# Kernel tuning notes

Hardware: AMD Instinct MI355X
Metric: run time of the kernel (lower is better)

Reference implementation:

```python
import math
import jax, jax.numpy as jnp
import numpy as np

B, T, D, H, L = 8, 512, 128, 128, 2
W_SCALE = 0.05  # xavier-like small init to keep exp() input gate numerically sane


def setup_inputs() -> dict:
    key = jax.random.key(0)
    ks = jax.random.split(key, 14)
    inp = {"x": jax.random.normal(ks[0], (B, T, D), jnp.float32)}
    names_w = ["Wq", "Wk", "Wv", "Wi", "Wf", "Wo"]
    for j, nm in enumerate(names_w):
        inp[nm] = jax.random.normal(ks[1 + j], (L, H, D), jnp.float32) * W_SCALE
    # q/k/v biases zero-initialized per reset_parameters; gate biases random
    inp["bq"] = jnp.zeros((L, H), jnp.float32)
    inp["bk"] = jnp.zeros((L, H), jnp.float32)
    inp["bv"] = jnp.zeros((L, H), jnp.float32)
    inp["bi"] = jax.random.normal(ks[7], (L, H), jnp.float32) * W_SCALE
    inp["bf"] = jax.random.normal(ks[8], (L, H), jnp.float32) * W_SCALE
    inp["bo"] = jax.random.normal(ks[9], (L, H), jnp.float32) * W_SCALE
    return inp


def _mlstm_layer(xin, Wq, bq, Wk, bk, Wv, bv, Wi, bi, Wf, bf, Wo, bo):
    # xin: (B, T, Din). Precompute all 6 projections for the full sequence.
    q = jnp.einsum("btd,hd->bth", xin, Wq) + bq
    k = (jnp.einsum("btd,hd->bth", xin, Wk) + bk) * (1.0 / math.sqrt(H))
    v = jnp.einsum("btd,hd->bth", xin, Wv) + bv
    i = jnp.exp(jnp.einsum("btd,hd->bth", xin, Wi) + bi)
    f = jax.nn.sigmoid(jnp.einsum("btd,hd->bth", xin, Wf) + bf)
    o = jax.nn.sigmoid(jnp.einsum("btd,hd->bth", xin, Wo) + bo)

    def step(carry, qkvifo):
        C, n = carry                      # C: (B,H,H), n: (B,H)
        qt, kt, vt, it, ft, ot = qkvifo   # each (B,H)
        h_tilde = jnp.einsum("bij,bj->bi", C, qt)
        denom = jnp.maximum(jnp.abs(jnp.einsum("bi,bi->b", n, qt)), 1.0)[:, None]
        h = ot * (h_tilde / denom)
        n_new = ft * n + it * kt
        C_new = ft[:, :, None] * C + it[:, :, None] * (vt[:, :, None] * kt[:, None, :])
        return (C_new, n_new), h

    Bc = xin.shape[0]
    C0 = jnp.zeros((Bc, H, H), xin.dtype)
    n0 = jnp.zeros((Bc, H), xin.dtype)
    seq = tuple(jnp.swapaxes(a, 0, 1) for a in (q, k, v, i, f, o))  # (T,B,H)
    _, hs = jax.lax.scan(step, (C0, n0), seq)
    return jnp.swapaxes(hs, 0, 1)  # (B,T,H)


def reference(x, Wq, bq, Wk, bk, Wv, bv, Wi, bi, Wf, bf, Wo, bo):
    h = x
    for l in range(L):  # small fixed layer loop (dropout=0.0 -> identity)
        h = _mlstm_layer(h, Wq[l], bq[l], Wk[l], bk[l], Wv[l], bv[l],
                         Wi[l], bi[l], Wf[l], bf[l], Wo[l], bo[l])
    return h  # (B, T, H) output sequence of last layer
```

## Files before the change

kernel.cpp:

```cpp
#include <hip/hip_runtime.h>
#include <math.h>

#define BB 8
#define TT 512
#define DD 128
#define HH 128
#define BT_ (BB * TT)
#define CL 32
#define NCH 16
static const size_t BTH = (size_t)BT_ * HH;


struct WArgs { const float* W[6]; };
struct BArgs { const float* b[6]; };

template <int CTRL>
__device__ __forceinline__ float dpp_add(float x) {
  int y = __builtin_amdgcn_update_dpp(0, __builtin_bit_cast(int, x), CTRL,
                                      0xF, 0xF, true);
  return x + __builtin_bit_cast(float, y);
}

__global__ __launch_bounds__(256)
void transpose_w(WArgs w, float* __restrict__ Wt) {
  __shared__ float t[32][33];
  const int l = blockIdx.y / 6, p = blockIdx.y % 6;
  const float* src = w.W[p] + (size_t)l * HH * DD;
  float* dst = Wt + (size_t)blockIdx.y * HH * DD;
  const int ty0 = (blockIdx.x >> 2) * 32, tx0 = (blockIdx.x & 3) * 32;
  const int tx = threadIdx.x & 31, ty = threadIdx.x >> 5;
#pragma unroll
  for (int j = 0; j < 32; j += 8)
    t[ty + j][tx] = src[(size_t)(ty0 + ty + j) * DD + tx0 + tx];
  __syncthreads();
#pragma unroll
  for (int j = 0; j < 32; j += 8)
    dst[(size_t)(tx0 + ty + j) * HH + ty0 + tx] = t[tx][ty + j];
}

__global__ __launch_bounds__(256)
void proj_kernel(const float* __restrict__ X, const float* __restrict__ Wtl,
                 BArgs args, float* __restrict__ act) {
  __shared__ float xs[64][132];
  const int p = blockIdx.y;
  const int row0 = blockIdx.x * 64;
  const int tid = threadIdx.x;
  {
    const float4* xg = (const float4*)(X + (size_t)row0 * DD);
#pragma unroll
    for (int i = 0; i < 8; ++i) {
      int u = tid + 256 * i;
      float4 v = xg[u];
      *(float4*)&xs[u >> 5][(u & 31) * 4] = v;
    }
  }
  __syncthreads();

  const int h0 = (tid & 15) * 8;
  const int r0 = (tid >> 4) * 4;
  const float* wtp = Wtl + (size_t)p * HH * DD;

  float acc[4][8];
#pragma unroll
  for (int r = 0; r < 4; ++r)
#pragma unroll
    for (int j = 0; j < 8; ++j) acc[r][j] = 0.f;

  for (int d0 = 0; d0 < DD; d0 += 4) {
    float4 wa[4], wb[4];
#pragma unroll
    for (int i = 0; i < 4; ++i) {
      wa[i] = *(const float4*)(wtp + (size_t)(d0 + i) * HH + h0);
      wb[i] = *(const float4*)(wtp + (size_t)(d0 + i) * HH + h0 + 4);
    }
    float4 xr[4];
#pragma unroll
    for (int r = 0; r < 4; ++r) xr[r] = *(const float4*)&xs[r0 + r][d0];
#pragma unroll
    for (int i = 0; i < 4; ++i) {
#pragma unroll
      for (int r = 0; r < 4; ++r) {
        const float xv = (i == 0) ? xr[r].x
                        : (i == 1) ? xr[r].y
                        : (i == 2) ? xr[r].z : xr[r].w;
        acc[r][0] = fmaf(xv, wa[i].x, acc[r][0]);
        acc[r][1] = fmaf(xv, wa[i].y, acc[r][1]);
        acc[r][2] = fmaf(xv, wa[i].z, acc[r][2]);
        acc[r][3] = fmaf(xv, wa[i].w, acc[r][3]);
        acc[r][4] = fmaf(xv, wb[i].x, acc[r][4]);
        acc[r][5] = fmaf(xv, wb[i].y, acc[r][5]);
        acc[r][6] = fmaf(xv, wb[i].z, acc[r][6]);
        acc[r][7] = fmaf(xv, wb[i].w, acc[r][7]);
      }
    }
  }

  const float4 b0 = *(const float4*)(args.b[p] + h0);
  const float4 b1 = *(const float4*)(args.b[p] + h0 + 4);
  const float bias[8] = {b0.x, b0.y, b0.z, b0.w, b1.x, b1.y, b1.z, b1.w};
#pragma unroll
  for (int r = 0; r < 4; ++r) {
    const size_t row = (size_t)row0 + r0 + r;
    float v[8];
#pragma unroll
    for (int j = 0; j < 8; ++j) {
      float a = acc[r][j] + bias[j];
      if (p == 1)      a *= 0.088388347648318447f;
      else if (p == 3) a = __expf(a);
      else if (p >= 4) a = 1.0f / (1.0f + __expf(-a));
      v[j] = a;
    }
    if (p == 0) {
      float* dst = act + row * HH + h0;
      *(float4*)dst = make_float4(v[0], v[1], v[2], v[3]);
      *(float4*)(dst + 4) = make_float4(v[4], v[5], v[6], v[7]);
    } else if (p == 1) {
      float* dst = act + BTH + row * HH + h0;
      *(float4*)dst = make_float4(v[0], v[1], v[2], v[3]);
      *(float4*)(dst + 4) = make_float4(v[4], v[5], v[6], v[7]);
    } else if (p == 3 || p == 4) {
      float* dst = act + 2 * BTH + row * 2 * HH + 2 * h0 + (p == 3 ? 0 : 1);
#pragma unroll
      for (int j = 0; j < 8; ++j) dst[2 * j] = v[j];
    } else {
      float* dst = act + 4 * BTH + row * 2 * HH + 2 * h0 + (p == 2 ? 0 : 1);
#pragma unroll
      for (int j = 0; j < 8; ++j) dst[2 * j] = v[j];
    }
  }
}

__global__ __launch_bounds__(512)
void cseg2_kernel(const float* __restrict__ act, float* __restrict__ cbuf,
                  float* __restrict__ abuf, float* __restrict__ nbufB) {
  __shared__ __align__(16) float kt[CL][128];
  __shared__ __align__(16) float ift[CL][64];
  __shared__ __align__(16) float vot[CL][64];
  const int tid = threadIdx.x;
  const int lane = tid & 63, wid = tid >> 6;
  const int blk = blockIdx.x;
  const int b = blk & 7, ch = (blk >> 3) & (NCH - 1), qtr = blk >> 7;
  const int t0 = ch * CL;
  const int p0 = qtr * 32;
  const size_t boff = (size_t)b * TT * HH;
  const float* kg = act + BTH + boff;
  const float* ifg = act + 2 * BTH + 2 * boff;
  const float* vog = act + 4 * BTH + 2 * boff;

#pragma unroll
  for (int i = 0; i < CL / 16; ++i) {
    const int u = tid + 512 * i;
    const int r = u >> 5, c = (u & 31) * 4;
    *(float4*)&kt[r][c] = *(const float4*)(kg + (size_t)(t0 + r) * HH + c);
  }
  {
    const int r = tid >> 4, c = (tid & 15) * 4;
    *(float4*)&ift[r][c] =
        *(const float4*)(ifg + (size_t)(t0 + r) * 2 * HH + 2 * p0 + c);
    *(float4*)&vot[r][c] =
        *(const float4*)(vog + (size_t)(t0 + r) * 2 * HH + 2 * p0 + c);
  }
  __syncthreads();

  const int pl = lane >> 4, cl = lane & 15;
  const int plocal = wid * 4 + pl;
  const int p = p0 + plocal;

  float C[8];
#pragma unroll
  for (int j = 0; j < 8; ++j) C[j] = 0.f;
  float Af = 1.f, Bn = 0.f;

#pragma unroll 4
  for (int t = 0; t < CL; ++t) {
    const float2 gif = *(const float2*)&ift[t][2 * plocal];
    const float2 gvo = *(const float2*)&vot[t][2 * plocal];
    const float4 k0 = *(const float4*)&kt[t][cl * 4];
    const float4 k1 = *(const float4*)&kt[t][cl * 4 + 64];
    const float kp = kt[t][p];
    const float a = gif.x * gvo.x;
    const float f = gif.y;
    C[0] = fmaf(f, C[0], a * k0.x);
    C[1] = fmaf(f, C[1], a * k0.y);
    C[2] = fmaf(f, C[2], a * k0.z);
    C[3] = fmaf(f, C[3], a * k0.w);
    C[4] = fmaf(f, C[4], a * k1.x);
    C[5] = fmaf(f, C[5], a * k1.y);
    C[6] = fmaf(f, C[6], a * k1.z);
    C[7] = fmaf(f, C[7], a * k1.w);
    Af *= f;
    Bn = fmaf(f, Bn, gif.x * kp);
  }

  const size_t slot = (size_t)(b * 128 + p) * NCH + ch;
  *(float4*)(cbuf + slot * 128 + cl * 4) = make_float4(C[0], C[1], C[2], C[3]);
  *(float4*)(cbuf + slot * 128 + cl * 4 + 64) =
      make_float4(C[4], C[5], C[6], C[7]);
  if (cl == 0) {
    abuf[slot] = Af;
    nbufB[slot] = Bn;
  }
}

__global__ __launch_bounds__(128)
void ndenom_kernel(float* __restrict__ act, const float* __restrict__ abuf,
                   const float* __restrict__ nbufB) {
  __shared__ float plds[8][132];
  __shared__ float den[8];
  const int b = blockIdx.x & 7, ch = blockIdx.x >> 3;
  const int p = threadIdx.x;
  const size_t boff = (size_t)b * TT * HH;
  const float* qp = act + boff + p;
  const float* kp = act + BTH + boff + p;
  const float* ifp = act + 2 * BTH + 2 * boff + 2 * p;
  float* vop = act + 4 * BTH + 2 * boff;
  const size_t cb = (size_t)(b * 128 + p) * NCH;

  float n = 0.f;
#pragma unroll 1
  for (int g = 0; g < ch; ++g) n = fmaf(abuf[cb + g], n, nbufB[cb + g]);

#pragma unroll 1
  for (int grp = 0; grp < CL / 8; ++grp) {
    const int t0 = ch * CL + grp * 8;
    float prod[8];
#pragma unroll
    for (int j = 0; j < 8; ++j) {
      const float2 iff = *(const float2*)(ifp + (size_t)(t0 + j) * 2 * HH);
      const float kv = kp[(size_t)(t0 + j) * HH];
      const float qv = qp[(size_t)(t0 + j) * HH];
      prod[j] = n * qv;
      n = fmaf(iff.y, n, iff.x * kv);
    }
#pragma unroll
    for (int j = 0; j < 8; ++j) plds[j][p] = prod[j];
    __syncthreads();
    {
      const int j = p >> 4, c = p & 15;
      const float4 a = *(const float4*)&plds[j][c * 8];
      const float4 d = *(const float4*)&plds[j][c * 8 + 4];
      float s = ((a.x + a.y) + (a.z + a.w)) + ((d.x + d.y) + (d.z + d.w));
      s = dpp_add<0x111>(s);
      s = dpp_add<0x112>(s);
      s = dpp_add<0x114>(s);
      s = dpp_add<0x118>(s);
      if ((p & 15) == 15)
        den[j] = __builtin_amdgcn_rcpf(fmaxf(fabsf(s), 1.0f));
    }
    __syncthreads();
#pragma unroll
    for (int j = 0; j < 8; ++j)
      vop[(size_t)(t0 + j) * 2 * HH + 2 * p + 1] *= den[j];
  }
}

__global__ __launch_bounds__(512)
void hscan2_kernel(const float* __restrict__ act, float* __restrict__ hout,
                   const float* __restrict__ cbuf,
                   const float* __restrict__ abuf) {
  __shared__ __align__(16) float qt[CL][128];
  __shared__ __align__(16) float kt[CL][128];
  __shared__ __align__(16) float ift[CL][64];
  __shared__ __align__(16) float vot[CL][64];
  const int tid = threadIdx.x;
  const int lane = tid & 63, wid = tid >> 6;
  const int blk = blockIdx.x;
  const int b = blk & 7, ch = (blk >> 3) & (NCH - 1), qtr = blk >> 7;
  const int t0 = ch * CL;
  const int p0 = qtr * 32;
  const size_t boff = (size_t)b * TT * HH;
  const float* qg = act + boff;
  const float* kg = act + BTH + boff;
  const float* ifg = act + 2 * BTH + 2 * boff;
  const float* vog = act + 4 * BTH + 2 * boff;

#pragma unroll
  for (int i = 0; i < CL / 16; ++i) {
    const int u = tid + 512 * i;
    const int r = u >> 5, c = (u & 31) * 4;
    *(float4*)&qt[r][c] = *(const float4*)(qg + (size_t)(t0 + r) * HH + c);
    *(float4*)&kt[r][c] = *(const float4*)(kg + (size_t)(t0 + r) * HH + c);
  }
  {
    const int r = tid >> 4, c = (tid & 15) * 4;
    *(float4*)&ift[r][c] =
        *(const float4*)(ifg + (size_t)(t0 + r) * 2 * HH + 2 * p0 + c);
    *(float4*)&vot[r][c] =
        *(const float4*)(vog + (size_t)(t0 + r) * 2 * HH + 2 * p0 + c);
  }
  __syncthreads();

  const int pl = lane >> 4, cl = lane & 15;
  const int plocal = wid * 4 + pl;
  const int p = p0 + plocal;

  float C[8];
#pragma unroll
  for (int j = 0; j < 8; ++j) C[j] = 0.f;
  {
    const size_t cb = (size_t)(b * 128 + p) * NCH;
#pragma unroll 1
    for (int g = 0; g < ch; ++g) {
      const float a = abuf[cb + g];
      const float4 b0 = *(const float4*)(cbuf + (cb + g) * 128 + cl * 4);
      const float4 b1 = *(const float4*)(cbuf + (cb + g) * 128 + cl * 4 + 64);
      C[0] = fmaf(a, C[0], b0.x);
      C[1] = fmaf(a, C[1], b0.y);
      C[2] = fmaf(a, C[2], b0.z);
      C[3] = fmaf(a, C[3], b0.w);
      C[4] = fmaf(a, C[4], b1.x);
      C[5] = fmaf(a, C[5], b1.y);
      C[6] = fmaf(a, C[6], b1.z);
      C[7] = fmaf(a, C[7], b1.w);
    }
  }
  float* hbase = hout + boff + p;

#pragma unroll 4
  for (int t = 0; t < CL; ++t) {
    const float2 gif = *(const float2*)&ift[t][2 * plocal];
    const float2 gvo = *(const float2*)&vot[t][2 * plocal];
    const float4 q0 = *(const float4*)&qt[t][cl * 4];
    const float4 q1 = *(const float4*)&qt[t][cl * 4 + 64];
    const float4 k0 = *(const float4*)&kt[t][cl * 4];
    const float4 k1 = *(const float4*)&kt[t][cl * 4 + 64];
    float s0 = C[0] * q0.x;
    float s1 = C[4] * q1.x;
    s0 = fmaf(C[1], q0.y, s0);
    s1 = fmaf(C[5], q1.y, s1);
    s0 = fmaf(C[2], q0.z, s0);
    s1 = fmaf(C[6], q1.z, s1);
    s0 = fmaf(C[3], q0.w, s0);
    s1 = fmaf(C[7], q1.w, s1);
    float s = s0 + s1;
    const float a = gif.x * gvo.x;
    const float f = gif.y;
    C[0] = fmaf(f, C[0], a * k0.x);
    C[1] = fmaf(f, C[1], a * k0.y);
    C[2] = fmaf(f, C[2], a * k0.z);
    C[3] = fmaf(f, C[3], a * k0.w);
    C[4] = fmaf(f, C[4], a * k1.x);
    C[5] = fmaf(f, C[5], a * k1.y);
    C[6] = fmaf(f, C[6], a * k1.z);
    C[7] = fmaf(f, C[7], a * k1.w);
    s = dpp_add<0x111>(s);
    s = dpp_add<0x112>(s);
    s = dpp_add<0x114>(s);
    s = dpp_add<0x118>(s);
    if (cl == 15) hbase[(size_t)(t0 + t) * HH] = s * gvo.y;
  }
}

extern "C" void kernel_launch(void* const* d_in, const int* in_sizes, int n_in,
                              void* d_out, int out_size, void* d_ws,
                              size_t ws_size, hipStream_t stream) {
  (void)in_sizes; (void)n_in; (void)out_size; (void)ws_size;
  const float* x = (const float*)d_in[0];
  float* act = (float*)d_ws;
  float* hbuf = act + 6 * BTH;
  float* cbuf = act + 7 * BTH;
  float* abuf = cbuf + (size_t)1024 * NCH * 128;
  float* nbufB = abuf + (size_t)1024 * NCH;
  float* Wt = (float*)d_out;

  WArgs wa;
  for (int j = 0; j < 6; ++j) wa.W[j] = (const float*)d_in[1 + j];
  transpose_w<<<dim3(16, 12), 256, 0, stream>>>(wa, Wt);

  for (int l = 0; l < 2; ++l) {
    BArgs ba;
    for (int j = 0; j < 6; ++j)
      ba.b[j] = (const float*)d_in[7 + j] + (size_t)l * HH;
    const float* wtl = Wt + (size_t)l * 6 * HH * DD;
    const float* xin = (l == 0) ? x : hbuf;
    float* hdst = (l == 0) ? hbuf : (float*)d_out;
    proj_kernel<<<dim3(BT_ / 64, 6), 256, 0, stream>>>(xin, wtl, ba, act);
    cseg2_kernel<<<512, 512, 0, stream>>>(act, cbuf, abuf, nbufB);
    ndenom_kernel<<<128, 128, 0, stream>>>(act, abuf, nbufB);
    hscan2_kernel<<<512, 512, 0, stream>>>(act, hdst, cbuf, abuf);
  }
}
```

Baseline: 205.0 us.

## Fold normalizer denominator computation into the h-scan kernel

```diff
diff --git a/kernel.cpp b/kernel.cpp
--- a/kernel.cpp
+++ b/kernel.cpp
@@ -132,7 +132,8 @@
 
 __global__ __launch_bounds__(512)
 void cseg2_kernel(const float* __restrict__ act, float* __restrict__ cbuf,
-                  float* __restrict__ abuf, float* __restrict__ nbufB) {
+                  float* __restrict__ abuf, float* __restrict__ nbufB,
+                  float* __restrict__ segA8, float* __restrict__ segB8) {
   __shared__ __align__(16) float kt[CL][128];
   __shared__ __align__(16) float ift[CL][64];
   __shared__ __align__(16) float vot[CL][64];
@@ -169,7 +170,7 @@
   float C[8];
 #pragma unroll
   for (int j = 0; j < 8; ++j) C[j] = 0.f;
-  float Af = 1.f, Bn = 0.f;
+  float Af = 1.f, Bn = 0.f, Aw = 1.f, Bw = 0.f;
 
 #pragma unroll 4
   for (int t = 0; t < CL; ++t) {
@@ -190,6 +191,17 @@
     C[7] = fmaf(f, C[7], a * k1.w);
     Af *= f;
     Bn = fmaf(f, Bn, gif.x * kp);
+    Aw *= f;
+    Bw = fmaf(f, Bw, gif.x * kp);
+    if ((t & 7) == 7) {
+      if (cl == 0) {
+        const size_t si = (size_t)(ch * 4 + (t >> 3)) * 1024 + b * 128 + p;
+        segA8[si] = Aw;
+        segB8[si] = Bw;
+      }
+      Aw = 1.f;
+      Bw = 0.f;
+    }
   }
 
   const size_t slot = (size_t)(b * 128 + p) * NCH + ch;
@@ -197,71 +209,25 @@
   *(float4*)(cbuf + slot * 128 + cl * 4 + 64) =
       make_float4(C[4], C[5], C[6], C[7]);
   if (cl == 0) {
-    abuf[slot] = Af;
-    nbufB[slot] = Bn;
-  }
-}
-
-__global__ __launch_bounds__(128)
-void ndenom_kernel(float* __restrict__ act, const float* __restrict__ abuf,
-                   const float* __restrict__ nbufB) {
-  __shared__ float plds[8][132];
-  __shared__ float den[8];
-  const int b = blockIdx.x & 7, ch = blockIdx.x >> 3;
-  const int p = threadIdx.x;
-  const size_t boff = (size_t)b * TT * HH;
-  const float* qp = act + boff + p;
-  const float* kp = act + BTH + boff + p;
-  const float* ifp = act + 2 * BTH + 2 * boff + 2 * p;
-  float* vop = act + 4 * BTH + 2 * boff;
-  const size_t cb = (size_t)(b * 128 + p) * NCH;
-
-  float n = 0.f;
-#pragma unroll 1
-  for (int g = 0; g < ch; ++g) n = fmaf(abuf[cb + g], n, nbufB[cb + g]);
-
-#pragma unroll 1
-  for (int grp = 0; grp < CL / 8; ++grp) {
-    const int t0 = ch * CL + grp * 8;
-    float prod[8];
-#pragma unroll
-    for (int j = 0; j < 8; ++j) {
-      const float2 iff = *(const float2*)(ifp + (size_t)(t0 + j) * 2 * HH);
-      const float kv = kp[(size_t)(t0 + j) * HH];
-      const float qv = qp[(size_t)(t0 + j) * HH];
-      prod[j] = n * qv;
-      n = fmaf(iff.y, n, iff.x * kv);
-    }
-#pragma unroll
-    for (int j = 0; j < 8; ++j) plds[j][p] = prod[j];
-    __syncthreads();
-    {
-      const int j = p >> 4, c = p & 15;
-      const float4 a = *(const float4*)&plds[j][c * 8];
-      const float4 d = *(const float4*)&plds[j][c * 8 + 4];
-      float s = ((a.x + a.y) + (a.z + a.w)) + ((d.x + d.y) + (d.z + d.w));
-      s = dpp_add<0x111>(s);
-      s = dpp_add<0x112>(s);
-      s = dpp_add<0x114>(s);
-      s = dpp_add<0x118>(s);
-      if ((p & 15) == 15)
-        den[j] = __builtin_amdgcn_rcpf(fmaxf(fabsf(s), 1.0f));
-    }
-    __syncthreads();
-#pragma unroll
-    for (int j = 0; j < 8; ++j)
-      vop[(size_t)(t0 + j) * 2 * HH + 2 * p + 1] *= den[j];
+    const size_t ci = (size_t)ch * 1024 + b * 128 + p;
+    abuf[ci] = Af;
+    nbufB[ci] = Bn;
   }
 }
 
 __global__ __launch_bounds__(512)
-void hscan2_kernel(const float* __restrict__ act, float* __restrict__ hout,
+void hscan3_kernel(const float* __restrict__ act, float* __restrict__ hout,
                    const float* __restrict__ cbuf,
-                   const float* __restrict__ abuf) {
+                   const float* __restrict__ abuf,
+                   const float* __restrict__ nbufB,
+                   const float* __restrict__ segA8,
+                   const float* __restrict__ segB8) {
   __shared__ __align__(16) float qt[CL][128];
   __shared__ __align__(16) float kt[CL][128];
-  __shared__ __align__(16) float ift[CL][64];
+  __shared__ __align__(16) float iff[CL][256];
   __shared__ __align__(16) float vot[CL][64];
+  __shared__ float den_part[4][8][2];
+  __shared__ float den[CL];
   const int tid = threadIdx.x;
   const int lane = tid & 63, wid = tid >> 6;
   const int blk = blockIdx.x;
@@ -281,12 +247,80 @@
     *(float4*)&qt[r][c] = *(const float4*)(qg + (size_t)(t0 + r) * HH + c);
     *(float4*)&kt[r][c] = *(const float4*)(kg + (size_t)(t0 + r) * HH + c);
   }
+#pragma unroll
+  for (int i = 0; i < 4; ++i) {
+    const int u = tid + 512 * i;
+    const int r = u >> 6, c = (u & 63) * 4;
+    *(float4*)&iff[r][c] =
+        *(const float4*)(ifg + (size_t)(t0 + r) * 2 * HH + c);
+  }
   {
     const int r = tid >> 4, c = (tid & 15) * 4;
-    *(float4*)&ift[r][c] =
-        *(const float4*)(ifg + (size_t)(t0 + r) * 2 * HH + 2 * p0 + c);
     *(float4*)&vot[r][c] =
         *(const float4*)(vog + (size_t)(t0 + r) * 2 * HH + 2 * p0 + c);
+  }
+  __syncthreads();
+
+  {
+    const int seg = tid >> 7, pd = tid & 127;
+    const size_t cidx = (size_t)b * 128 + pd;
+    float av[NCH], bv[NCH];
+#pragma unroll
+    for (int g = 0; g < NCH; ++g) {
+      av[g] = abuf[(size_t)g * 1024 + cidx];
+      bv[g] = nbufB[(size_t)g * 1024 + cidx];
+    }
+    float a8[3], b8[3];
+#pragma unroll
+    for (int s = 0; s < 3; ++s) {
+      const size_t si = (size_t)(ch * 4 + s) * 1024 + cidx;
+      a8[s] = segA8[si];
+      b8[s] = segB8[si];
+    }
+    float n = 0.f;
+#pragma unroll
+    for (int g = 0; g < NCH; ++g)
+      if (g < ch) n = fmaf(av[g], n, bv[g]);
+#pragma unroll
+    for (int s = 0; s < 3; ++s)
+      if (s < seg) n = fmaf(a8[s], n, b8[s]);
+    float prod[8];
+#pragma unroll
+    for (int j = 0; j < 8; ++j) {
+      const int tl = seg * 8 + j;
+      const float iv = iff[tl][2 * pd];
+      const float fv = iff[tl][2 * pd + 1];
+      prod[j] = n * qt[tl][pd];
+      n = fmaf(fv, n, iv * kt[tl][pd]);
+    }
+#pragma unroll
+    for (int j = 0; j < 8; ++j) {
+      float s = prod[j];
+      s = dpp_add<0x111>(s);
+      s = dpp_add<0x112>(s);
+      s = dpp_add<0x114>(s);
+      s = dpp_add<0x118>(s);
+      s = dpp_add<0x142>(s);
+      s = dpp_add<0x143>(s);
+      prod[j] = s;
+    }
+    if (lane == 63) {
+#pragma unroll
+      for (int j = 0; j < 8; ++j) den_part[seg][j][wid & 1] = prod[j];
+    }
+  }
+  __syncthreads();
+  if (tid < CL) {
+    const int s_ = tid >> 3, j_ = tid & 7;
+    const float d = den_part[s_][j_][0] + den_part[s_][j_][1];
+    den[tid] = __builtin_amdgcn_rcpf(fmaxf(fabsf(d), 1.0f));
+  }
+  __syncthreads();
+  {
+    int u = tid;
+    vot[u >> 5][2 * (u & 31) + 1] *= den[u >> 5];
+    u = tid + 512;
+    vot[u >> 5][2 * (u & 31) + 1] *= den[u >> 5];
   }
   __syncthreads();
 
@@ -301,7 +335,7 @@
     const size_t cb = (size_t)(b * 128 + p) * NCH;
 #pragma unroll 1
     for (int g = 0; g < ch; ++g) {
-      const float a = abuf[cb + g];
+      const float a = abuf[(size_t)g * 1024 + b * 128 + p];
       const float4 b0 = *(const float4*)(cbuf + (cb + g) * 128 + cl * 4);
       const float4 b1 = *(const float4*)(cbuf + (cb + g) * 128 + cl * 4 + 64);
       C[0] = fmaf(a, C[0], b0.x);
@@ -318,7 +352,7 @@
 
 #pragma unroll 4
   for (int t = 0; t < CL; ++t) {
-    const float2 gif = *(const float2*)&ift[t][2 * plocal];
+    const float2 gif = *(const float2*)&iff[t][2 * p];
     const float2 gvo = *(const float2*)&vot[t][2 * plocal];
     const float4 q0 = *(const float4*)&qt[t][cl * 4];
     const float4 q1 = *(const float4*)&qt[t][cl * 4 + 64];
@@ -360,7 +394,9 @@
   float* hbuf = act + 6 * BTH;
   float* cbuf = act + 7 * BTH;
   float* abuf = cbuf + (size_t)1024 * NCH * 128;
-  float* nbufB = abuf + (size_t)1024 * NCH;
+  float* nbufB = abuf + 16384;
+  float* segA8 = nbufB + 16384;
+  float* segB8 = segA8 + 65536;
   float* Wt = (float*)d_out;
 
   WArgs wa;
@@ -375,8 +411,9 @@
     const float* xin = (l == 0) ? x : hbuf;
     float* hdst = (l == 0) ? hbuf : (float*)d_out;
     proj_kernel<<<dim3(BT_ / 64, 6), 256, 0, stream>>>(xin, wtl, ba, act);
-    cseg2_kernel<<<512, 512, 0, stream>>>(act, cbuf, abuf, nbufB);
-    ndenom_kernel<<<128, 128, 0, stream>>>(act, abuf, nbufB);
-    hscan2_kernel<<<512, 512, 0, stream>>>(act, hdst, cbuf, abuf);
-  }
-}
+    cseg2_kernel<<<512, 512, 0, stream>>>(act, cbuf, abuf, nbufB, segA8,
+                                          segB8);
+    hscan3_kernel<<<512, 512, 0, stream>>>(act, hdst, cbuf, abuf, nbufB,
+                                           segA8, segB8);
+  }
+}
```

After: 198.0 us (median of 2 runs). 3.4% less time.
